# Kernel optimization log

Hardware: AMD Instinct MI355X
Metric: run time of the kernel (lower is better)

Reference implementation:

```python
import jax, jax.numpy as jnp
import numpy as np


def _grid_sample_bilinear(img, grid):
    # img: [N, C, H, W]; grid: [N, Ho, Wo, 2] (x,y) in [-1,1]
    # matches torch.nn.functional.grid_sample(mode='bilinear', padding_mode='zeros', align_corners=False)
    N, C, H, W = img.shape
    Ho, Wo = grid.shape[1], grid.shape[2]
    ix = (grid[..., 0] + 1.0) * (W * 0.5) - 0.5  # unnormalize, align_corners=False
    iy = (grid[..., 1] + 1.0) * (H * 0.5) - 0.5
    x0 = jnp.floor(ix)
    y0 = jnp.floor(iy)
    x1 = x0 + 1.0
    y1 = y0 + 1.0
    wx1 = ix - x0
    wx0 = 1.0 - wx1
    wy1 = iy - y0
    wy0 = 1.0 - wy1
    img_flat = img.reshape(N, C, H * W)

    def corner(xf, yf, w):
        valid = (xf >= 0) & (xf <= W - 1) & (yf >= 0) & (yf <= H - 1)
        xi = jnp.clip(xf.astype(jnp.int32), 0, W - 1)
        yi = jnp.clip(yf.astype(jnp.int32), 0, H - 1)
        idx = (yi * W + xi).reshape(N, 1, Ho * Wo)
        vals = jnp.take_along_axis(img_flat, idx, axis=2)  # [N, C, Ho*Wo]
        wv = (w * valid.astype(img.dtype)).reshape(N, 1, Ho * Wo)
        return vals * wv

    out = (corner(x0, y0, wx0 * wy0) + corner(x1, y0, wx1 * wy0)
           + corner(x0, y1, wx0 * wy1) + corner(x1, y1, wx1 * wy1))
    return out.reshape(N, C, Ho, Wo)


def setup_inputs() -> dict:
    key = jax.random.key(0)
    k1, k2 = jax.random.split(key)
    B, L, C, H, W = 2, 24, 16, 64, 64
    flows = jax.random.normal(k1, (B, L, 2, H, W), dtype=jnp.float32) * 0.01
    images = jax.random.normal(k2, (B, L, C, H, W), dtype=jnp.float32)
    return {"flows": flows, "images": images}


def reference(flows, images):
    B, L, _, H, W = flows.shape
    C = images.shape[2]
    dtype = flows.dtype
    cum_flows = jnp.cumsum(flows.astype(jnp.float32), axis=1).astype(dtype)  # [B,L,2,H,W]
    k_idx, t_idx = np.triu_indices(L)  # all pairs k <= t, N_pairs = L(L+1)/2
    N_pairs = k_idx.size
    # relative flow from frame k to frame t for every pair
    rel = (cum_flows[:, t_idx] - cum_flows[:, k_idx])  # [B, N_pairs, 2, H, W]
    rel = rel.reshape(B * N_pairs, 2, H, W).transpose(0, 2, 3, 1)  # [BN, H, W, 2]
    # pixel-center base grid (align_corners=False convention)
    gy = jnp.linspace(-1.0 + 1.0 / H, 1.0 - 1.0 / H, H, dtype=dtype)
    gx = jnp.linspace(-1.0 + 1.0 / W, 1.0 - 1.0 / W, W, dtype=dtype)
    base = jnp.stack(jnp.meshgrid(gx, gy, indexing='xy'), axis=-1)  # [H, W, 2] (x,y)
    grid = base[None] + rel
    # wrap x coordinate into [-1, 1)
    grid = grid.at[..., 0].set(jnp.remainder(grid[..., 0] + 1.0, 2.0) - 1.0)
    flat_images = images[:, k_idx].reshape(B * N_pairs, C, H, W)
    warped = _grid_sample_bilinear(flat_images, grid)  # [BN, C, H, W]
    targets = (np.arange(B)[:, None] * L + t_idx[None, :]).reshape(-1)
    out = jax.ops.segment_sum(warped, jnp.asarray(targets), num_segments=B * L)
    return out.reshape(B, L, C, H, W)
```

## Files before the change

kernel.cpp:

```cpp
#include <hip/hip_runtime.h>


#define BB 2
#define LL 24
#define CC 16
#define HH 64
#define WW 64
#define HW (HH * WW)
#define NW 6
#define CAP 12
#define CHS (CAP * WW)

__device__ __forceinline__ void bilin_coords(
    float gxv0, float gyv,
    int& x0c, int& x1c, int& y0c, int& y1c,
    float& w00, float& w10, float& w01, float& w11)
{
    const float v = gxv0 + 1.0f;
    float r = v - 2.0f * truncf(v * 0.5f);
    r = (r < 0.0f) ? (r + 2.0f) : r;
    const float gxv = r - 1.0f;

    const float ix = (gxv + 1.0f) * 32.0f - 0.5f;
    const float iy = (gyv + 1.0f) * 32.0f - 0.5f;

    const float x0f = floorf(ix);
    const float y0f = floorf(iy);
    const float x1f = x0f + 1.0f;
    const float y1f = y0f + 1.0f;

    const float wx1 = ix - x0f, wx0 = 1.0f - wx1;
    const float wy1 = iy - y0f, wy0 = 1.0f - wy1;

    const bool vx0 = (x0f >= 0.0f) && (x0f <= 63.0f);
    const bool vx1 = (x1f >= 0.0f) && (x1f <= 63.0f);
    const bool vy0 = (y0f >= 0.0f) && (y0f <= 63.0f);
    const bool vy1 = (y1f >= 0.0f) && (y1f <= 63.0f);

    x0c = min(max((int)x0f, 0), WW - 1);
    x1c = min(max((int)x1f, 0), WW - 1);
    y0c = min(max((int)y0f, 0), HH - 1);
    y1c = min(max((int)y1f, 0), HH - 1);

    w00 = (vx0 && vy0) ? (wx0 * wy0) : 0.0f;
    w10 = (vx1 && vy0) ? (wx1 * wy0) : 0.0f;
    w01 = (vx0 && vy1) ? (wx0 * wy1) : 0.0f;
    w11 = (vx1 && vy1) ? (wx1 * wy1) : 0.0f;
}

__global__ __launch_bounds__(NW * 64, 4) void gsps_band(
    const float* __restrict__ flows,
    const float* __restrict__ images,
    float* __restrict__ out)
{
    __shared__ float lds[CC * CHS];
    __shared__ int bandW[NW];

    const int bid = blockIdx.x;
    const int y_hi = bid & 7;
    int u = bid >> 3;
    const int y_lo = u & 7; u >>= 3;
    const int q = u & 3;
    const int b = u >> 2;
    const int y = (y_hi << 3) | y_lo;
    const int lane = threadIdx.x & 63;
    const int w = threadIdx.x >> 6;
    const int t = q + 4 * w;
    const int kmax = q + 20;

    const float gx = -0.984375f + (float)lane * 0.03125f;
    const float gy = -0.984375f + (float)y * 0.03125f;
    const int pix = y * WW + lane;
    const float* fb = flows + (size_t)b * LL * 2 * HW + pix;

    float ctx = 0.0f, cty = 0.0f;
    for (int i = 0; i <= t; ++i) {
        ctx += fb[(size_t)(2 * i) * HW];
        cty += fb[(size_t)(2 * i + 1) * HW];
    }

    float acc[CC];
#pragma unroll
    for (int c = 0; c < CC; ++c) acc[c] = 0.0f;

    float cx = 0.0f, cy = 0.0f;
    float fkx = fb[0], fky = fb[HW];
    const int lg = lane >> 4;
    const int li = lane & 15;

    for (int k = 0; k <= kmax; ++k) {
        cx += fkx; cy += fky;
        if (k < kmax) {
            fkx = fb[(size_t)(2 * (k + 1)) * HW];
            fky = fb[(size_t)(2 * (k + 1) + 1) * HW];
        }

        const bool act = (t >= k);
        int x0c = 0, x1c = 0, y0c = 0, y1c = 0;
        float w00 = 0.f, w10 = 0.f, w01 = 0.f, w11 = 0.f;
        if (act)
            bilin_coords(gx + (ctx - cx), gy + (cty - cy),
                         x0c, x1c, y0c, y1c, w00, w10, w01, w11);

        int ymn = act ? y0c : 64;
        int ymx = act ? y1c : -1;
#pragma unroll
        for (int m = 1; m < 64; m <<= 1) {
            ymn = min(ymn, __shfl_xor(ymn, m));
            ymx = max(ymx, __shfl_xor(ymx, m));
        }
        if (lane == 0) bandW[w] = (ymn << 8) | (ymx + 1);
        __syncthreads();

        int lo = 64, hx = 0;
#pragma unroll
        for (int ww = 0; ww < NW; ++ww) {
            const int bv = bandW[ww];
            lo = min(lo, bv >> 8);
            hx = max(hx, bv & 255);
        }
        const int nrows = hx - lo;
        const bool fbk = nrows > CAP;

        const float* imgk = images + (size_t)(b * LL + k) * (CC * HW);

        if (!fbk) {
            const int nslots = nrows * 4;
            for (int slot = w; slot < nslots; slot += NW) {
                const int seg = slot * 4 + lg;
                const int c = seg & (CC - 1);
                const int r = seg >> 4;
                const float4 vv = *(const float4*)(imgk + (size_t)c * HW
                                                   + (lo + r) * WW + li * 4);
                *(float4*)&lds[c * CHS + r * WW + li * 4] = vv;
            }
        }
        __syncthreads();

        if (act) {
            if (!fbk) {
                const int a0 = (y0c - lo) * WW + x0c;
                const int a1 = (y0c - lo) * WW + x1c;
                const int b0 = (y1c - lo) * WW + x0c;
                const int b1 = (y1c - lo) * WW + x1c;
#pragma unroll
                for (int c = 0; c < CC; ++c) {
                    const float* s = lds + c * CHS;
                    acc[c] += s[a0] * w00 + s[a1] * w10 + s[b0] * w01 + s[b1] * w11;
                }
            } else {
                const int g00 = y0c * WW + x0c, g10 = y0c * WW + x1c;
                const int g01 = y1c * WW + x0c, g11 = y1c * WW + x1c;
#pragma unroll
                for (int c = 0; c < CC; ++c) {
                    const float* pc = imgk + (size_t)c * HW;
                    acc[c] += pc[g00] * w00 + pc[g10] * w10 + pc[g01] * w01 + pc[g11] * w11;
                }
            }
        }
    }

    float* o = out + ((size_t)(b * LL + t) * CC) * HW + pix;
#pragma unroll
    for (int c = 0; c < CC; ++c) o[(size_t)c * HW] = acc[c];
}

extern "C" void kernel_launch(void* const* d_in, const int* in_sizes, int n_in,
                              void* d_out, int out_size, void* d_ws, size_t ws_size,
                              hipStream_t stream) {
    const float* flows  = (const float*)d_in[0];
    const float* images = (const float*)d_in[1];
    float* out = (float*)d_out;

    const int nblk = BB * 4 * HH;
    gsps_band<<<nblk, NW * 64, 0, stream>>>(flows, images, out);
}
```

Measured before the change: 138.6 us.

## Use fixed LDS row window with register-prefetched next frame staging

Swaps the per-iteration dynamic band computation (wave shuffles plus an extra barrier) for a fixed 12-row window centred on the block's row. The next frame's window is prefetched into registers while the current frame is sampled, then written to LDS after a barrier, so global load latency overlaps compute. Corner pairs are loaded as adjacent columns with remapped weights to simplify addressing. This raises register pressure (occupancy hint drops from 4 to 3) and always loads the full window even when fewer rows are needed; out-of-window samples still fall back to global loads.

```diff
diff --git a/kernel.cpp b/kernel.cpp
--- a/kernel.cpp
+++ b/kernel.cpp
@@ -8,53 +8,15 @@
 #define WW 64
 #define HW (HH * WW)
 #define NW 6
-#define CAP 12
-#define CHS (CAP * WW)
+#define WROWS 12
+#define CHS (WROWS * WW)
 
-__device__ __forceinline__ void bilin_coords(
-    float gxv0, float gyv,
-    int& x0c, int& x1c, int& y0c, int& y1c,
-    float& w00, float& w10, float& w01, float& w11)
-{
-    const float v = gxv0 + 1.0f;
-    float r = v - 2.0f * truncf(v * 0.5f);
-    r = (r < 0.0f) ? (r + 2.0f) : r;
-    const float gxv = r - 1.0f;
-
-    const float ix = (gxv + 1.0f) * 32.0f - 0.5f;
-    const float iy = (gyv + 1.0f) * 32.0f - 0.5f;
-
-    const float x0f = floorf(ix);
-    const float y0f = floorf(iy);
-    const float x1f = x0f + 1.0f;
-    const float y1f = y0f + 1.0f;
-
-    const float wx1 = ix - x0f, wx0 = 1.0f - wx1;
-    const float wy1 = iy - y0f, wy0 = 1.0f - wy1;
-
-    const bool vx0 = (x0f >= 0.0f) && (x0f <= 63.0f);
-    const bool vx1 = (x1f >= 0.0f) && (x1f <= 63.0f);
-    const bool vy0 = (y0f >= 0.0f) && (y0f <= 63.0f);
-    const bool vy1 = (y1f >= 0.0f) && (y1f <= 63.0f);
-
-    x0c = min(max((int)x0f, 0), WW - 1);
-    x1c = min(max((int)x1f, 0), WW - 1);
-    y0c = min(max((int)y0f, 0), HH - 1);
-    y1c = min(max((int)y1f, 0), HH - 1);
-
-    w00 = (vx0 && vy0) ? (wx0 * wy0) : 0.0f;
-    w10 = (vx1 && vy0) ? (wx1 * wy0) : 0.0f;
-    w01 = (vx0 && vy1) ? (wx0 * wy1) : 0.0f;
-    w11 = (vx1 && vy1) ? (wx1 * wy1) : 0.0f;
-}
-
-__global__ __launch_bounds__(NW * 64, 4) void gsps_band(
+__global__ __launch_bounds__(NW * 64, 3) void gsps_fixw(
     const float* __restrict__ flows,
     const float* __restrict__ images,
     float* __restrict__ out)
 {
     __shared__ float lds[CC * CHS];
-    __shared__ int bandW[NW];
 
     const int bid = blockIdx.x;
     const int y_hi = bid & 7;
@@ -67,6 +29,10 @@
     const int w = threadIdx.x >> 6;
     const int t = q + 4 * w;
     const int kmax = q + 20;
+    const int lg = lane >> 4;
+    const int li = lane & 15;
+
+    const int wlo = min(max(y - 5, 0), HH - WROWS);
 
     const float gx = -0.984375f + (float)lane * 0.03125f;
     const float gy = -0.984375f + (float)y * 0.03125f;
@@ -85,8 +51,24 @@
 
     float cx = 0.0f, cy = 0.0f;
     float fkx = fb[0], fky = fb[HW];
-    const int lg = lane >> 4;
-    const int li = lane & 15;
+
+    {
+        const float* img0 = images + (size_t)(b * LL) * (CC * HW);
+        float4 st[8];
+#pragma unroll
+        for (int s = 0; s < 8; ++s) {
+            const int slot = w + s * NW;
+            const int c = slot & 15, rg = slot >> 4;
+            st[s] = *(const float4*)(img0 + (size_t)c * HW + (wlo + rg * 4 + lg) * WW + li * 4);
+        }
+#pragma unroll
+        for (int s = 0; s < 8; ++s) {
+            const int slot = w + s * NW;
+            const int c = slot & 15, rg = slot >> 4;
+            *(float4*)&lds[c * CHS + (rg * 4 + lg) * WW + li * 4] = st[s];
+        }
+    }
+    __syncthreads();
 
     for (int k = 0; k <= kmax; ++k) {
         cx += fkx; cy += fky;
@@ -95,60 +77,71 @@
             fky = fb[(size_t)(2 * (k + 1) + 1) * HW];
         }
 
-        const bool act = (t >= k);
-        int x0c = 0, x1c = 0, y0c = 0, y1c = 0;
-        float w00 = 0.f, w10 = 0.f, w01 = 0.f, w11 = 0.f;
-        if (act)
-            bilin_coords(gx + (ctx - cx), gy + (cty - cy),
-                         x0c, x1c, y0c, y1c, w00, w10, w01, w11);
-
-        int ymn = act ? y0c : 64;
-        int ymx = act ? y1c : -1;
+        float4 st[8];
+        if (k < kmax) {
+            const float* imgn = images + (size_t)(b * LL + k + 1) * (CC * HW);
 #pragma unroll
-        for (int m = 1; m < 64; m <<= 1) {
-            ymn = min(ymn, __shfl_xor(ymn, m));
-            ymx = max(ymx, __shfl_xor(ymx, m));
-        }
-        if (lane == 0) bandW[w] = (ymn << 8) | (ymx + 1);
-        __syncthreads();
-
-        int lo = 64, hx = 0;
-#pragma unroll
-        for (int ww = 0; ww < NW; ++ww) {
-            const int bv = bandW[ww];
-            lo = min(lo, bv >> 8);
-            hx = max(hx, bv & 255);
-        }
-        const int nrows = hx - lo;
-        const bool fbk = nrows > CAP;
-
-        const float* imgk = images + (size_t)(b * LL + k) * (CC * HW);
-
-        if (!fbk) {
-            const int nslots = nrows * 4;
-            for (int slot = w; slot < nslots; slot += NW) {
-                const int seg = slot * 4 + lg;
-                const int c = seg & (CC - 1);
-                const int r = seg >> 4;
-                const float4 vv = *(const float4*)(imgk + (size_t)c * HW
-                                                   + (lo + r) * WW + li * 4);
-                *(float4*)&lds[c * CHS + r * WW + li * 4] = vv;
+            for (int s = 0; s < 8; ++s) {
+                const int slot = w + s * NW;
+                const int c = slot & 15, rg = slot >> 4;
+                st[s] = *(const float4*)(imgn + (size_t)c * HW + (wlo + rg * 4 + lg) * WW + li * 4);
             }
         }
-        __syncthreads();
 
+        const bool act = (t >= k);
         if (act) {
-            if (!fbk) {
-                const int a0 = (y0c - lo) * WW + x0c;
-                const int a1 = (y0c - lo) * WW + x1c;
-                const int b0 = (y1c - lo) * WW + x0c;
-                const int b1 = (y1c - lo) * WW + x1c;
+            const float relx = ctx - cx, rely = cty - cy;
+            const float v = (gx + relx) + 1.0f;
+            float r = v - 2.0f * truncf(v * 0.5f);
+            r = (r < 0.0f) ? (r + 2.0f) : r;
+            const float gxv = r - 1.0f;
+            const float gyv = gy + rely;
+
+            const float ix = (gxv + 1.0f) * 32.0f - 0.5f;
+            const float iy = (gyv + 1.0f) * 32.0f - 0.5f;
+
+            const float x0f = floorf(ix), y0f = floorf(iy);
+            const float x1f = x0f + 1.0f, y1f = y0f + 1.0f;
+            const float wx1 = ix - x0f, wx0 = 1.0f - wx1;
+            const float wy1 = iy - y0f, wy0 = 1.0f - wy1;
+
+            const bool vx0 = (x0f >= 0.0f) && (x0f <= 63.0f);
+            const bool vx1 = (x1f >= 0.0f) && (x1f <= 63.0f);
+            const bool vy0 = (y0f >= 0.0f) && (y0f <= 63.0f);
+            const bool vy1 = (y1f >= 0.0f) && (y1f <= 63.0f);
+
+            const int x0c = min(max((int)x0f, 0), WW - 1);
+            const int x1c = min(max((int)x1f, 0), WW - 1);
+            const int y0c = min(max((int)y0f, 0), HH - 1);
+            const int y1c = min(max((int)y1f, 0), HH - 1);
+
+            const float w00 = (vx0 && vy0) ? (wx0 * wy0) : 0.0f;
+            const float w10 = (vx1 && vy0) ? (wx1 * wy0) : 0.0f;
+            const float w01 = (vx0 && vy1) ? (wx0 * wy1) : 0.0f;
+            const float w11 = (vx1 && vy1) ? (wx1 * wy1) : 0.0f;
+
+            const bool flb = (y0c < wlo) || (y1c > wlo + (WROWS - 1));
+
+            if (!flb) {
+                const int p = min(max((int)x0f, 0), WW - 2);
+                const bool e0 = (x0c == p);
+                const bool e1 = (x1c == p);
+                const float wA0 = (e0 ? w00 : 0.0f) + (e1 ? w10 : 0.0f);
+                const float wA1 = (e0 ? 0.0f : w00) + (e1 ? 0.0f : w10);
+                const float wB0 = (e0 ? w01 : 0.0f) + (e1 ? w11 : 0.0f);
+                const float wB1 = (e0 ? 0.0f : w01) + (e1 ? 0.0f : w11);
+                const int baseA = (y0c - wlo) * WW + p;
+                const int baseB = (y1c - wlo) * WW + p;
 #pragma unroll
                 for (int c = 0; c < CC; ++c) {
-                    const float* s = lds + c * CHS;
-                    acc[c] += s[a0] * w00 + s[a1] * w10 + s[b0] * w01 + s[b1] * w11;
+                    const float vA0 = lds[c * CHS + baseA];
+                    const float vA1 = lds[c * CHS + baseA + 1];
+                    const float vB0 = lds[c * CHS + baseB];
+                    const float vB1 = lds[c * CHS + baseB + 1];
+                    acc[c] += vA0 * wA0 + vA1 * wA1 + vB0 * wB0 + vB1 * wB1;
                 }
             } else {
+                const float* imgk = images + (size_t)(b * LL + k) * (CC * HW);
                 const int g00 = y0c * WW + x0c, g10 = y0c * WW + x1c;
                 const int g01 = y1c * WW + x0c, g11 = y1c * WW + x1c;
 #pragma unroll
@@ -158,6 +151,17 @@
                 }
             }
         }
+
+        __syncthreads();
+        if (k < kmax) {
+#pragma unroll
+            for (int s = 0; s < 8; ++s) {
+                const int slot = w + s * NW;
+                const int c = slot & 15, rg = slot >> 4;
+                *(float4*)&lds[c * CHS + (rg * 4 + lg) * WW + li * 4] = st[s];
+            }
+        }
+        __syncthreads();
     }
 
     float* o = out + ((size_t)(b * LL + t) * CC) * HW + pix;
@@ -173,5 +177,5 @@
     float* out = (float*)d_out;
 
     const int nblk = BB * 4 * HH;
-    gsps_band<<<nblk, NW * 64, 0, stream>>>(flows, images, out);
+    gsps_fixw<<<nblk, NW * 64, 0, stream>>>(flows, images, out);
 }
```

Measured after the change: 249.5 us. +80.0%, slower.
